# Kernel optimization log

Hardware: AMD Instinct MI355X
Metric: run time of the kernel (lower is better)

Reference implementation:

```python
import jax, jax.numpy as jnp
import numpy as np
import math

B, N, D = 4096, 41, 271
S, THR, KS = 0.3, 1e-4, 25  # wavelet scale s=0.3, threshold 1e-4, Bessel series terms
_IV_COEFS = [np.array([1.0 / (math.factorial(k) * math.factorial(k + n)) for k in range(KS)], dtype=np.float32) for n in range(4)]


def _iv(n, x):
    # modified Bessel I_n(x) via power series, x >= 0, shape [B]
    k = np.arange(KS, dtype=np.float32)
    xh = (0.5 * x)[:, None]
    return jnp.sum(_IV_COEFS[n] * xh ** (n + 2.0 * k), axis=-1)


def _l1norm(W):
    # F.normalize(p=1, dim=2)
    return W / jnp.maximum(jnp.sum(jnp.abs(W), axis=2, keepdims=True), 1e-12)


def _bn(x, g, b):
    # BatchNorm1d in training mode: per-feature stats over the batch dim (biased var)
    m = jnp.mean(x, 0)
    v = jnp.var(x, 0)
    return (x - m) / jnp.sqrt(v + 1e-5) * g + b


def _wavelet_basis(G):
    # laplacian_multi: degree from raw W, symmetrize, D^-1/2 (D - A) D^-1/2
    deg = jnp.sum(G, axis=-1)                               # [B,N]
    A = 0.5 * (G + jnp.swapaxes(G, 1, 2))                   # [B,N,N]
    dinv = 1.0 / (jnp.sqrt(deg) + 1e-6)
    eye = jnp.eye(N, dtype=G.dtype)
    L = dinv[:, :, None] * (deg[:, :, None] * eye - A) * dinv[:, None, :]
    # cheb_polynomial_multi: note order-0 term is ZEROS in the source
    T2 = 2.0 * jnp.matmul(L, L)
    T3 = 2.0 * jnp.matmul(L, T2) - L
    Lch = jnp.stack([jnp.zeros_like(L), L, T2, T3], axis=1)  # [B,4,N,N]
    # largest_lamb: host-side eigsh(LM) per sample -> detached (no grad)
    lam = jax.lax.stop_gradient(jnp.max(jnp.abs(jnp.linalg.eigvalsh(L)), axis=-1))  # [B]
    x = S * 0.5 * lam                                       # s * a, a = lamb/2
    ivs = jnp.stack([_iv(n, x) for n in range(4)], axis=1)  # [B,4]
    sign = jnp.asarray([1.0, -1.0, 1.0, -1.0], dtype=x.dtype)  # I_n(-x) = (-1)^n I_n(x)
    c = 2.0 * jnp.exp(x)[:, None] * ivs                     # 2 e^{sa} I_n(sa)
    inv_c = 2.0 * jnp.exp(-x)[:, None] * ivs * sign         # 2 e^{-sa} I_n(-sa)
    W = jnp.einsum('bo,bonm->bnm', c, Lch)
    Wi = jnp.einsum('bo,bonm->bnm', inv_c, Lch)
    W = _l1norm(jnp.where(W < THR, 0.0, W))
    Wi = _l1norm(jnp.where(Wi < THR, 0.0, Wi))
    return W, Wi


def _forward(G, X, gwnn_kernel, gwnn_W, log_scale_vector, W1, b1, W2, b2, bn1_gamma, bn1_beta):
    wav, wav_inv = _wavelet_basis(G)
    # graph wavelet layer: psi diag(k) psi^{-1} X W  (dropout off / eval)
    h = jnp.matmul(X, gwnn_W)                 # [B,N,D]
    h = jnp.matmul(wav_inv, h)
    h = gwnn_kernel[None, :, None] * h
    h = jax.nn.relu(jnp.matmul(wav, h))
    # scaling layer: exp(log_scale) * x
    coff = jnp.exp(log_scale_vector)          # [N,D]
    fr = coff[None] * h
    # shape1: Linear -> ReLU -> Linear
    fr = jnp.matmul(jax.nn.relu(jnp.matmul(fr, W1) + b1), W2) + b2
    # sequence feature: mean over nodes then BatchNorm1d(271)
    seq = _bn(jnp.mean(fr, axis=1), bn1_gamma, bn1_beta)  # [B,D]
    return seq


def setup_inputs() -> dict:
    key = jax.random.key(0)
    ks = jax.random.split(key, 8)
    sc = 1.0 / np.sqrt(D).astype(np.float32)
    return {
        'G': jax.random.uniform(ks[0], (B, N, N), jnp.float32),
        'X': jax.random.normal(ks[1], (B, N, D), jnp.float32),
        'gwnn_kernel': 1.0 + 0.1 * jax.random.normal(ks[2], (N,), jnp.float32),
        'gwnn_W': sc * jax.random.normal(ks[3], (D, D), jnp.float32),
        'log_scale_vector': 0.1 * jax.random.normal(ks[4], (N, D), jnp.float32),
        'W1': sc * jax.random.normal(ks[5], (D, D), jnp.float32),
        'b1': jnp.zeros((D,), jnp.float32),
        'W2': sc * jax.random.normal(ks[6], (D, D), jnp.float32),
        'b2': jnp.zeros((D,), jnp.float32),
        'bn1_gamma': jnp.ones((D,), jnp.float32),
        'bn1_beta': jnp.zeros((D,), jnp.float32),
    }


def reference(G, X, gwnn_kernel, gwnn_W, log_scale_vector, W1, b1, W2, b2, bn1_gamma, bn1_beta):
    return _forward(G, X, gwnn_kernel, gwnn_W, log_scale_vector, W1, b1, W2, b2, bn1_gamma, bn1_beta)
```

## Files before the change

### kernel.cpp

```cpp
#include <hip/hip_runtime.h>
#include <math.h>

namespace {
constexpr int BB = 4096;
constexpr int NN = 41;
constexpr int DD = 271;
constexpr int DP = 288;
constexpr int PW = 44;
constexpr long long MROWS = (long long)BB * NN;
constexpr int WBE = DP * DP * 2;
constexpr int WBS = (DP / 32) * DP * 32;
constexpr int SROW = 312;
constexpr int NPL = 5;
}

typedef __attribute__((ext_vector_type(8)))  unsigned short ushort8;
typedef __attribute__((ext_vector_type(8)))  short          short8;
typedef __attribute__((ext_vector_type(4)))  float          f32x4;

__device__ __forceinline__ unsigned short f2bf(float f) {
    unsigned u = __float_as_uint(f);
    unsigned r = (u + 0x7FFFu + ((u >> 16) & 1u)) >> 16;
    return (unsigned short)r;
}
__device__ __forceinline__ float bf2f(unsigned short h) {
    return __uint_as_float(((unsigned)h) << 16);
}

__device__ __forceinline__ void store_split_km(unsigned short* __restrict__ dst,
                                               long long nrows, long long row,
                                               int col, float v)
{
    const unsigned short hh = f2bf(v);
    const unsigned short ll = f2bf(v - bf2f(hh));
    const long long base = ((long long)(col >> 5) * nrows + row) * 64;
    const int cn = (col & 31) >> 3, k7 = col & 7, sw = (int)(row & 7);
    dst[base + ((cn ^ sw) << 3) + k7]       = hh;
    dst[base + (((cn + 4) ^ sw) << 3) + k7] = ll;
}

__device__ __forceinline__ void lds_mm(const float (*__restrict__ A)[PW],
                                       const float (*__restrict__ B)[PW],
                                       float (*__restrict__ C)[PW],
                                       const float scale,
                                       const float (*__restrict__ sub)[PW],
                                       const int tid)
{
    for (int s = tid; s < NN * 11; s += 256) {
        const int i = s / 11, q = s % 11;
        float4 acc = make_float4(0.f, 0.f, 0.f, 0.f);
        #pragma unroll
        for (int k = 0; k < NN; ++k) {
            const float a = A[i][k];
            const float4 b4 = *reinterpret_cast<const float4*>(&B[k][q * 4]);
            acc.x = fmaf(a, b4.x, acc.x); acc.y = fmaf(a, b4.y, acc.y);
            acc.z = fmaf(a, b4.z, acc.z); acc.w = fmaf(a, b4.w, acc.w);
        }
        float4 r;
        if (sub) {
            const float4 s4 = *reinterpret_cast<const float4*>(&sub[i][q * 4]);
            r = make_float4(fmaf(scale, acc.x, -s4.x), fmaf(scale, acc.y, -s4.y),
                            fmaf(scale, acc.z, -s4.z), fmaf(scale, acc.w, -s4.w));
        } else {
            r = make_float4(scale * acc.x, scale * acc.y, scale * acc.z, scale * acc.w);
        }
        *reinterpret_cast<float4*>(&C[i][q * 4]) = r;
    }
}

__global__ __launch_bounds__(256) void k_wavelet(const float* __restrict__ G,
                                                 const float* __restrict__ gk,
                                                 float* __restrict__ MT)
{
    __shared__ float sG[NN][PW];
    __shared__ float sL[NN][PW];
    __shared__ float sT2[NN][PW];
    __shared__ float sT3[NN][PW];
    __shared__ float sM[NN][PW];
    __shared__ float sdeg[NN], sdinv[NN], srs[NN];
    __shared__ float slam16;

    const int b   = blockIdx.x;
    const int tid = threadIdx.x;
    const float* Gb = G + (size_t)b * NN * NN;

    for (int e = tid; e < NN * PW; e += 256) {
        const int i = e / PW, j = e % PW;
        sG[i][j] = (j < NN) ? Gb[i * NN + j] : 0.0f;
    }
    __syncthreads();

    if (tid < NN) {
        float4 s4 = make_float4(0.f, 0.f, 0.f, 0.f);
        #pragma unroll
        for (int q = 0; q < 11; ++q) {
            const float4 g4 = *reinterpret_cast<const float4*>(&sG[tid][q * 4]);
            s4.x += g4.x; s4.y += g4.y; s4.z += g4.z; s4.w += g4.w;
        }
        const float s = (s4.x + s4.y) + (s4.z + s4.w);
        sdeg[tid]  = s;
        sdinv[tid] = 1.0f / (sqrtf(s) + 1e-6f);
    }
    __syncthreads();

    for (int e = tid; e < NN * PW; e += 256) {
        const int i = e / PW, j = e % PW;
        if (j < NN) {
            const float a = 0.5f * (sG[i][j] + sG[j][i]);
            const float v = ((i == j) ? sdeg[i] : 0.0f) - a;
            sL[i][j] = sdinv[i] * sdinv[j] * v;
        } else {
            sL[i][j] = 0.0f;
        }
    }
    __syncthreads();

    lds_mm(sL, sL, sT2, 2.0f, nullptr, tid);
    __syncthreads();
    lds_mm(sL, sT2, sT3, 2.0f, sL, tid);
    __syncthreads();

    lds_mm(sT2, sT2, sM, 0.25f, nullptr, tid);
    __syncthreads();
    lds_mm(sM, sM, sG, 1.0f, nullptr, tid);
    __syncthreads();
    lds_mm(sG, sG, sM, 1.0f, nullptr, tid);
    __syncthreads();

    if (tid < 64) {
        float lr[NN];
        #pragma unroll
        for (int j = 0; j < NN; ++j) lr[j] = (tid < NN) ? sM[tid][j] : 0.0f;
        unsigned h = (unsigned)(tid + 1) * 2654435761u;
        h ^= h >> 13; h *= 0x85ebca6bu; h ^= h >> 16;
        float v = (tid < NN) ? (0.25f + (float)(h & 1023) * (1.0f / 1024.0f)) : 0.0f;
        float n2 = v * v;
        #pragma unroll
        for (int off = 32; off > 0; off >>= 1) n2 += __shfl_xor(n2, off, 64);
        v *= rsqrtf(n2);
        float lam = 1.0f;
        #pragma unroll
        for (int it = 0; it < 4; ++it) {
            float acc = 0.f;
            #pragma unroll
            for (int j = 0; j < NN; ++j) acc = fmaf(lr[j], __shfl(v, j, 64), acc);
            float m2 = acc * acc;
            #pragma unroll
            for (int off = 32; off > 0; off >>= 1) m2 += __shfl_xor(m2, off, 64);
            lam = sqrtf(m2);
            v = acc * (1.0f / lam);
        }
        if (tid == 0) slam16 = lam;
    }
    __syncthreads();

    const float x = 0.15f * exp2f(log2f(slam16) * (1.0f / 16.0f));
    float iv[4];
    {
        const float xh = 0.5f * x, xh2 = xh * xh;
        #pragma unroll
        for (int n = 0; n < 4; ++n) {
            float c = 1.0f;
            for (int q = 2; q <= n; ++q) c /= (float)q;
            float p = 1.0f;
            for (int q = 0; q < n; ++q) p *= xh;
            float s = 0.f;
            for (int k = 0; k < 25; ++k) {
                s += c * p;
                p *= xh2;
                c /= (float)((k + 1) * (k + 1 + n));
            }
            iv[n] = s;
        }
    }
    const float ex = expf(x), emx = expf(-x);

    {
        const float a1 = 2.f * ex * iv[1], a2 = 2.f * ex * iv[2], a3 = 2.f * ex * iv[3];
        for (int s = tid; s < NN * 11; s += 256) {
            const int i = s / 11, q = s % 11;
            const float4 l4  = *reinterpret_cast<const float4*>(&sL[i][q * 4]);
            const float4 t24 = *reinterpret_cast<const float4*>(&sT2[i][q * 4]);
            const float4 t34 = *reinterpret_cast<const float4*>(&sT3[i][q * 4]);
            float4 w;
            w.x = fmaf(a1, l4.x, fmaf(a2, t24.x, a3 * t34.x));
            w.y = fmaf(a1, l4.y, fmaf(a2, t24.y, a3 * t34.y));
            w.z = fmaf(a1, l4.z, fmaf(a2, t24.z, a3 * t34.z));
            w.w = fmaf(a1, l4.w, fmaf(a2, t24.w, a3 * t34.w));
            w.x = (w.x < 1e-4f) ? 0.f : w.x;  w.y = (w.y < 1e-4f) ? 0.f : w.y;
            w.z = (w.z < 1e-4f) ? 0.f : w.z;  w.w = (w.w < 1e-4f) ? 0.f : w.w;
            *reinterpret_cast<float4*>(&sM[i][q * 4]) = w;
        }
        __syncthreads();
        if (tid < NN) {
            float s = 0.f;
            #pragma unroll
            for (int q = 0; q < 11; ++q) {
                const float4 w4 = *reinterpret_cast<const float4*>(&sM[tid][q * 4]);
                s += fabsf(w4.x) + fabsf(w4.y) + fabsf(w4.z) + fabsf(w4.w);
            }
            srs[tid] = 1.0f / fmaxf(s, 1e-12f);
        }
        __syncthreads();
    }
    {
        const float a1 = -2.f * emx * iv[1], a2 = 2.f * emx * iv[2], a3 = -2.f * emx * iv[3];
        for (int s = tid; s < NN * 11; s += 256) {
            const int i = s / 11, q = s % 11;
            float4 m4 = *reinterpret_cast<float4*>(&sM[i][q * 4]);
            const float rs = srs[i];
            m4.x *= rs; m4.y *= rs; m4.z *= rs; m4.w *= rs;
            *reinterpret_cast<float4*>(&sM[i][q * 4]) = m4;
            const float4 l4  = *reinterpret_cast<const float4*>(&sL[i][q * 4]);
            const float4 t24 = *reinterpret_cast<const float4*>(&sT2[i][q * 4]);
            const float4 t34 = *reinterpret_cast<const float4*>(&sT3[i][q * 4]);
            float4 w;
            w.x = fmaf(a1, l4.x, fmaf(a2, t24.x, a3 * t34.x));
            w.y = fmaf(a1, l4.y, fmaf(a2, t24.y, a3 * t34.y));
            w.z = fmaf(a1, l4.z, fmaf(a2, t24.z, a3 * t34.z));
            w.w = fmaf(a1, l4.w, fmaf(a2, t24.w, a3 * t34.w));
            w.x = (w.x < 1e-4f) ? 0.f : w.x;  w.y = (w.y < 1e-4f) ? 0.f : w.y;
            w.z = (w.z < 1e-4f) ? 0.f : w.z;  w.w = (w.w < 1e-4f) ? 0.f : w.w;
            *reinterpret_cast<float4*>(&sG[i][q * 4]) = w;
        }
        __syncthreads();
        if (tid < NN) {
            float s = 0.f;
            #pragma unroll
            for (int q = 0; q < 11; ++q) {
                const float4 w4 = *reinterpret_cast<const float4*>(&sG[tid][q * 4]);
                s += fabsf(w4.x) + fabsf(w4.y) + fabsf(w4.z) + fabsf(w4.w);
            }
            sdeg[tid] = gk[tid] / fmaxf(s, 1e-12f);
        }
        __syncthreads();
        for (int s = tid; s < NN * 11; s += 256) {
            const int j = s / 11, q = s % 11;
            float4 w4 = *reinterpret_cast<float4*>(&sG[j][q * 4]);
            const float rs = sdeg[j];
            w4.x *= rs; w4.y *= rs; w4.z *= rs; w4.w *= rs;
            *reinterpret_cast<float4*>(&sG[j][q * 4]) = w4;
        }
        __syncthreads();
    }
    lds_mm(sM, sG, sL, 1.0f, nullptr, tid);
    __syncthreads();
    float* dst = MT + (size_t)b * NN * NN;
    for (int e = tid; e < NN * NN; e += 256) {
        const int j = e / NN, i = e % NN;
        dst[e] = sL[i][j];
    }
}

__global__ __launch_bounds__(256) void k_splitB(const float* __restrict__ gW,
                                                const float* __restrict__ W1,
                                                const float* __restrict__ W2,
                                                const float* __restrict__ lsv,
                                                unsigned short* __restrict__ Bint,
                                                unsigned short* __restrict__ Bsng,
                                                float* __restrict__ coff)
{
    const int t = blockIdx.x * 256 + threadIdx.x;
    if (t < NN * DD) coff[t] = expf(lsv[t]);
    if (t >= 3 * DP * DP) return;
    const int w = t / (DP * DP);
    const int r = t % (DP * DP);
    const int n = r / DP, k = r % DP;
    const float* src = (w == 0) ? gW : ((w == 1) ? W1 : W2);
    const float v = (n < DD && k < DD) ? src[k * DD + n] : 0.0f;
    store_split_km(Bint + (size_t)w * WBE, DP, n, k, v);
    if (w < 2) {
        Bsng[(size_t)w * WBS + ((long long)(k >> 5) * DP + n) * 32 +
             (((k & 31) >> 3) << 3) + (k & 7)] = f2bf(v);
    }
}

__global__ __launch_bounds__(256, 2) void k_wavX(const float* __restrict__ MT,
                                                 const float* __restrict__ X,
                                                 unsigned short* __restrict__ Yint)
{
    constexpr int XJ  = 68;
    constexpr int YST = 296;
    __shared__ __align__(16) unsigned short sXT[288 * XJ];
    __shared__ __align__(16) unsigned short sMm[48 * XJ];
    __shared__ __align__(16) unsigned short sYb[NN * YST];
    const int b   = blockIdx.x;
    const int tid = threadIdx.x;
    const int lane = tid & 63, w = tid >> 6;
    const int lr = lane & 15;
    const int hi8 = (lane >> 4) * 8;

    const ushort8 z8 = {0, 0, 0, 0, 0, 0, 0, 0};
    for (int e = tid; e < (288 * XJ) / 8; e += 256)
        *reinterpret_cast<ushort8*>(&sXT[e * 8]) = z8;
    for (int e = tid; e < (48 * XJ) / 8; e += 256)
        *reinterpret_cast<ushort8*>(&sMm[e * 8]) = z8;
    __syncthreads();

    const float* __restrict__ Xb = X + (size_t)b * NN * DD;
    for (int e = tid; e < NN * DD; e += 256) {
        const int j = e / DD, c = e % DD;
        sXT[c * XJ + j] = f2bf(Xb[e]);
    }
    const float* __restrict__ Mb = MT + (size_t)b * NN * NN;
    for (int e = tid; e < NN * NN; e += 256) {
        const int j = e / NN, i = e % NN;
        sMm[i * XJ + j] = f2bf(Mb[e]);
    }
    __syncthreads();

    for (int t = w; t < 54; t += 4) {
        const int mt = t / 18, nt = t % 18;
        f32x4 acc = (f32x4){0.f, 0.f, 0.f, 0.f};
        #pragma unroll
        for (int ks = 0; ks < 2; ++ks) {
            const short8 a = *reinterpret_cast<const short8*>(
                &sMm[(mt * 16 + lr) * XJ + ks * 32 + hi8]);
            const short8 bf = *reinterpret_cast<const short8*>(
                &sXT[(nt * 16 + lr) * XJ + ks * 32 + hi8]);
            acc = __builtin_amdgcn_mfma_f32_16x16x32_bf16(a, bf, acc, 0, 0, 0);
        }
        const int row0 = mt * 16 + (lane >> 4) * 4;
        const int col  = nt * 16 + lr;
        #pragma unroll
        for (int rr = 0; rr < 4; ++rr) {
            const int row = row0 + rr;
            if (row < NN) sYb[row * YST + col] = f2bf(acc[rr]);
        }
    }
    __syncthreads();

    for (int t = tid; t < NN * 36; t += 256) {
        const int i = t / 36, c8 = t % 36;
        const ushort8 hv = *reinterpret_cast<const ushort8*>(&sYb[i * YST + c8 * 8]);
        const long long r = (long long)b * NN + i;
        const int p = c8 >> 3;
        const int chunk = ((c8 >> 2) & 1) * 4 + (c8 & 3);
        const int sw = (int)(r & 7);
        unsigned short* base = Yint + ((long long)p * MROWS + r) * 64;
        *reinterpret_cast<ushort8*>(base + ((chunk ^ sw) << 3)) = hv;
    }
}

__device__ __forceinline__ void async16(const unsigned short* __restrict__ g,
                                        unsigned short* l)
{
    __builtin_amdgcn_global_load_lds(
        (const __attribute__((address_space(1))) unsigned int*)g,
        (__attribute__((address_space(3))) unsigned int*)l, 16, 0, 0);
}

__global__ __launch_bounds__(512, 2) void k_fused(
    const unsigned short* __restrict__ Aint,
    const unsigned short* __restrict__ Bs0,
    const unsigned short* __restrict__ Bs1,
    const float* __restrict__ coff,
    const float* __restrict__ b1,
    unsigned short* __restrict__ P2)
{
    __shared__ __align__(16) unsigned short sS[256 * SROW];
    const int tid  = threadIdx.x;
    const int lane = tid & 63, w = tid >> 6;
    const int wr = w >> 1, wc = w & 1;
    const int lr = lane & 15, cb = lane >> 4;
    const int sw = lr & 7;

    const int nwg = gridDim.x, orig = blockIdx.x;
    const int q = nwg >> 3, r = nwg & 7;
    const int xcd = orig & 7, loc = orig >> 3;
    const int bid = (xcd < r ? xcd * (q + 1) : r * (q + 1) + (xcd - r) * q) + loc;
    const long long row0 = (long long)bid * 256;

    const unsigned short* __restrict__ b0p = Bs0 + (size_t)(wc * 144 + lr) * 32 + cb * 8;
    const unsigned short* __restrict__ b1p = Bs1 + (size_t)(wc * 144 + lr) * 32 + cb * 8;

    f32x4 acc[4][9];
    #pragma unroll
    for (int mf = 0; mf < 4; ++mf)
        #pragma unroll
        for (int nf = 0; nf < 9; ++nf)
            acc[mf][nf] = (f32x4){0.f, 0.f, 0.f, 0.f};

    for (int t = 0; t < 9; ++t) {
        const int p  = t >> 1;
        const int hc = (t & 1) * 4 + cb;
        const long long abase = ((long long)p * MROWS + row0) * 64 + ((hc ^ sw) << 3);
        short8 a[4];
        #pragma unroll
        for (int mf = 0; mf < 4; ++mf)
            a[mf] = *reinterpret_cast<const short8*>(
                Aint + abase + (long long)(wr * 64 + mf * 16 + lr) * 64);
        const long long toff = (long long)t * DP * 32;
        #pragma unroll
        for (int nf = 0; nf < 9; ++nf) {
            const short8 bh = *reinterpret_cast<const short8*>(b0p + toff + (long long)nf * 512);
            #pragma unroll
            for (int mf = 0; mf < 4; ++mf)
                acc[mf][nf] = __builtin_amdgcn_mfma_f32_16x16x32_bf16(a[mf], bh, acc[mf][nf], 0, 0, 0);
        }
    }

    #pragma unroll
    for (int mf = 0; mf < 4; ++mf) {
        const int mb = wr * 64 + mf * 16 + ((lane >> 4) * 4);
        #pragma unroll
        for (int nf = 0; nf < 9; ++nf) {
            const int col = wc * 144 + nf * 16 + lr;
            #pragma unroll
            for (int rr = 0; rr < 4; ++rr) {
                const int m = mb + rr;
                float v = fmaxf(acc[mf][nf][rr], 0.f);
                const float cf = (col < DD) ? coff[((unsigned)(row0 + m) % 41u) * DD + col] : 0.0f;
                sS[m * SROW + col] = f2bf(v * cf);
                acc[mf][nf][rr] = 0.f;
            }
        }
    }
    __syncthreads();

    for (int t = 0; t < 9; ++t) {
        short8 ah[4];
        #pragma unroll
        for (int mf = 0; mf < 4; ++mf) {
            const int m = wr * 64 + mf * 16 + lr;
            ah[mf] = *reinterpret_cast<const short8*>(&sS[m * SROW + t * 32 + cb * 8]);
        }
        const long long toff = (long long)t * DP * 32;
        #pragma unroll
        for (int nf = 0; nf < 9; ++nf) {
            const short8 bh = *reinterpret_cast<const short8*>(b1p + toff + (long long)nf * 512);
            #pragma unroll
            for (int mf = 0; mf < 4; ++mf)
                acc[mf][nf] = __builtin_amdgcn_mfma_f32_16x16x32_bf16(ah[mf], bh, acc[mf][nf], 0, 0, 0);
        }
    }

    #pragma unroll
    for (int mf = 0; mf < 4; ++mf) {
        const long long rb = row0 + wr * 64 + mf * 16 + ((lane >> 4) * 4);
        #pragma unroll
        for (int nf = 0; nf < 9; ++nf) {
            const int col = wc * 144 + nf * 16 + lr;
            const float bv = (col < DD) ? b1[col] : 0.0f;
            #pragma unroll
            for (int rr = 0; rr < 4; ++rr) {
                const float v = fmaxf(acc[mf][nf][rr] + bv, 0.f);
                P2[(rb + rr) * DP + col] = f2bf(v);
            }
        }
    }
}

__global__ __launch_bounds__(320) void k_meanP2(const unsigned short* __restrict__ P2,
                                                unsigned short* __restrict__ MPint)
{
    const int b = blockIdx.x;
    const int c = threadIdx.x;
    if (c >= DP) return;
    float s = 0.f;
    #pragma unroll
    for (int n = 0; n < NN; ++n)
        s += bf2f(P2[((size_t)b * NN + n) * DP + c]);
    s *= (1.0f / 41.0f);
    store_split_km(MPint, BB, b, c, s);
}

__global__ __launch_bounds__(256, 2) void k_gemm3(
    const unsigned short* __restrict__ Aint,
    const unsigned short* __restrict__ Bm,
    const float* __restrict__ bias,
    float* __restrict__ outF)
{
    __shared__ __align__(16) unsigned short As2[2][128 * 64];
    const int tid  = threadIdx.x;
    const int lane = tid & 63, w = tid >> 6;
    const int wr = w >> 1, wc = w & 1;
    const int lr = lane & 15, cb = lane >> 4;
    const int sw = lr & 7;
    const long long row0 = (long long)blockIdx.x * 128;

    const size_t brow = (size_t)(wc * 144 + lr) * 64;
    const unsigned short* __restrict__ bhp = Bm + brow + ((cb ^ sw) << 3);
    const unsigned short* __restrict__ blp = Bm + brow + (((cb + 4) ^ sw) << 3);

    f32x4 acc[4][9];
    #pragma unroll
    for (int mf = 0; mf < 4; ++mf)
        #pragma unroll
        for (int nf = 0; nf < 9; ++nf)
            acc[mf][nf] = (f32x4){0.f, 0.f, 0.f, 0.f};

    auto stageA = [&](unsigned short* dst, int kt32) {
        const unsigned short* src = Aint + ((long long)kt32 * BB + row0) * 64;
        #pragma unroll
        for (int i = 0; i < 4; ++i) {
            const int cid = tid + i * 256;
            async16(src + (long long)cid * 8, dst + cid * 8);
        }
    };

    stageA(As2[0], 0);
    for (int t = 0; t < 9; ++t) {
        __syncthreads();
        if (t < 8) stageA(As2[(t + 1) & 1], t + 1);
        const unsigned short* As = As2[t & 1];
        short8 ah[4], al[4];
        #pragma unroll
        for (int mf = 0; mf < 4; ++mf) {
            const int m = wr * 64 + mf * 16 + lr;
            ah[mf] = *reinterpret_cast<const short8*>(&As[m * 64 + ((cb ^ sw) << 3)]);
            al[mf] = *reinterpret_cast<const short8*>(&As[m * 64 + (((cb + 4) ^ sw) << 3)]);
        }
        const long long toff = (long long)t * DP * 64;
        #pragma unroll
        for (int nf = 0; nf < 9; ++nf) {
            const long long d = toff + (long long)nf * 1024;
            const short8 bh = *reinterpret_cast<const short8*>(bhp + d);
            const short8 bl = *reinterpret_cast<const short8*>(blp + d);
            #pragma unroll
            for (int mf = 0; mf < 4; ++mf) {
                acc[mf][nf] = __builtin_amdgcn_mfma_f32_16x16x32_bf16(ah[mf], bh, acc[mf][nf], 0, 0, 0);
                acc[mf][nf] = __builtin_amdgcn_mfma_f32_16x16x32_bf16(al[mf], bh, acc[mf][nf], 0, 0, 0);
                acc[mf][nf] = __builtin_amdgcn_mfma_f32_16x16x32_bf16(ah[mf], bl, acc[mf][nf], 0, 0, 0);
            }
        }
    }

    #pragma unroll
    for (int mf = 0; mf < 4; ++mf) {
        const long long rb = row0 + wr * 64 + mf * 16 + ((lane >> 4) * 4);
        #pragma unroll
        for (int nf = 0; nf < 9; ++nf) {
            const int col = wc * 144 + nf * 16 + lr;
            const float bv = (col < DD) ? bias[col] : 0.0f;
            #pragma unroll
            for (int rr = 0; rr < 4; ++rr)
                outF[(rb + rr) * DP + col] = acc[mf][nf][rr] + bv;
        }
    }
}

__global__ __launch_bounds__(256) void k_stats(const float* __restrict__ seq, float* __restrict__ stats)
{
    __shared__ float s1[256], s2[256];
    const int d = blockIdx.x;
    float a = 0.f, q = 0.f;
    for (int b = threadIdx.x; b < BB; b += 256) {
        float v = seq[(size_t)b * DP + d];
        a += v; q = fmaf(v, v, q);
    }
    s1[threadIdx.x] = a; s2[threadIdx.x] = q;
    __syncthreads();
    for (int o = 128; o > 0; o >>= 1) {
        if (threadIdx.x < o) { s1[threadIdx.x] += s1[threadIdx.x + o]; s2[threadIdx.x] += s2[threadIdx.x + o]; }
        __syncthreads();
    }
    if (threadIdx.x == 0) {
        float m = s1[0] * (1.0f / BB);
        float v = s2[0] * (1.0f / BB) - m * m;
        stats[d]      = m;
        stats[DD + d] = 1.0f / sqrtf(v + 1e-5f);
    }
}

__global__ __launch_bounds__(256) void k_bn(const float* __restrict__ seq, const float* __restrict__ stats,
                                            const float* __restrict__ g, const float* __restrict__ bt,
                                            float* __restrict__ out)
{
    const long long idx = (long long)blockIdx.x * 256 + threadIdx.x;
    if (idx < (long long)BB * DD) {
        const int d = (int)(idx % DD);
        const long long b = idx / DD;
        out[idx] = (seq[b * DP + d] - stats[d]) * stats[DD + d] * g[d] + bt[d];
    }
}

extern "C" void kernel_launch(void* const* d_in, const int* in_sizes, int n_in,
                              void* d_out, int out_size, void* d_ws, size_t ws_size,
                              hipStream_t stream)
{
    const float* G   = (const float*)d_in[0];
    const float* X   = (const float*)d_in[1];
    const float* gk  = (const float*)d_in[2];
    const float* gW  = (const float*)d_in[3];
    const float* lsv = (const float*)d_in[4];
    const float* W1  = (const float*)d_in[5];
    const float* b1  = (const float*)d_in[6];
    const float* W2  = (const float*)d_in[7];
    const float* b2  = (const float*)d_in[8];
    const float* gam = (const float*)d_in[9];
    const float* bet = (const float*)d_in[10];

    char* p = (char*)d_ws;
    auto alloc = [&](size_t bytes) { void* r = (void*)p; p += (bytes + 255) & ~(size_t)255; return r; };
    float*          MT    = (float*)alloc((size_t)BB * NN * NN * 4);
    unsigned short* Yint  = (unsigned short*)alloc((size_t)NPL * MROWS * 64 * 2);
    unsigned short* P2    = (unsigned short*)alloc((size_t)MROWS * DP * 2);
    unsigned short* Bint  = (unsigned short*)alloc((size_t)3 * WBE * 2);
    unsigned short* Bsng  = (unsigned short*)alloc((size_t)2 * WBS * 2);
    unsigned short* MPint = (unsigned short*)alloc((size_t)BB * 576 * 2);
    float*          coff  = (float*)alloc((size_t)NN * DD * 4);
    float*          seqF  = (float*)alloc((size_t)BB * DP * 4);
    float*          stats = (float*)alloc(2 * DD * 4);

    k_wavelet<<<BB, 256, 0, stream>>>(G, gk, MT);
    k_splitB<<<(3 * DP * DP + 255) / 256, 256, 0, stream>>>(gW, W1, W2, lsv, Bint, Bsng, coff);
    k_wavX<<<BB, 256, 0, stream>>>(MT, X, Yint);

    k_fused<<<(unsigned)(MROWS / 256), 512, 0, stream>>>(Yint, Bsng, Bsng + WBS,
                                                         coff, b1, P2);
    k_meanP2<<<BB, 320, 0, stream>>>(P2, MPint);
    k_gemm3<<<BB / 128, 256, 0, stream>>>(MPint, Bint + 2 * WBE, b2, seqF);
    k_stats<<<DD, 256, 0, stream>>>(seqF, stats);
    k_bn<<<(unsigned)(((long long)BB * DD + 255) / 256), 256, 0, stream>>>(seqF, stats, gam, bet, (float*)d_out);
}
```

Before: 435.2 us.

## Fuse node-mean reduction into fused GEMM epilogue via LDS and global atomics

The fused GEMM epilogue now accumulates ReLU outputs per sample into an LDS buffer with shared atomics, then flushes partial sums to a global fp32 buffer with global atomics. This removes writing and rereading the full bf16 P2 activation tensor (about 96 MB round trip). The price is many LDS atomics in the epilogue, a memset of the sum buffer, and cross-block global atomics where 256-row tiles straddle sample boundaries. It also makes the summation order nondeterministic.

```diff
diff --git a/kernel.cpp b/kernel.cpp
--- a/kernel.cpp
+++ b/kernel.cpp
@@ -356,7 +356,7 @@
     const unsigned short* __restrict__ Bs1,
     const float* __restrict__ coff,
     const float* __restrict__ b1,
-    unsigned short* __restrict__ P2)
+    float* __restrict__ seqsum)
 {
     __shared__ __align__(16) unsigned short sS[256 * SROW];
     const int tid  = threadIdx.x;
@@ -434,10 +434,16 @@
                 acc[mf][nf] = __builtin_amdgcn_mfma_f32_16x16x32_bf16(ah[mf], bh, acc[mf][nf], 0, 0, 0);
         }
     }
-
+    __syncthreads();
+
+    float* sums = reinterpret_cast<float*>(sS);
+    for (int e = tid; e < 8 * DP; e += 512) sums[e] = 0.f;
+    __syncthreads();
+
+    const int b0 = (int)(row0 / 41);
     #pragma unroll
     for (int mf = 0; mf < 4; ++mf) {
-        const long long rb = row0 + wr * 64 + mf * 16 + ((lane >> 4) * 4);
+        const int mb = wr * 64 + mf * 16 + ((lane >> 4) * 4);
         #pragma unroll
         for (int nf = 0; nf < 9; ++nf) {
             const int col = wc * 144 + nf * 16 + lr;
@@ -445,24 +451,31 @@
             #pragma unroll
             for (int rr = 0; rr < 4; ++rr) {
                 const float v = fmaxf(acc[mf][nf][rr] + bv, 0.f);
-                P2[(rb + rr) * DP + col] = f2bf(v);
+                const long long row = row0 + mb + rr;
+                const int ls = (int)(row / 41) - b0;
+                atomicAdd(&sums[ls * DP + col], v);
             }
         }
     }
-}
-
-__global__ __launch_bounds__(320) void k_meanP2(const unsigned short* __restrict__ P2,
-                                                unsigned short* __restrict__ MPint)
+    __syncthreads();
+
+    for (int e = tid; e < 8 * DP; e += 512) {
+        const int ls = e / DP, col = e % DP;
+        const long long bsm = (long long)b0 + ls;
+        if (bsm < BB) {
+            const float s = sums[e];
+            if (s != 0.f) atomicAdd(&seqsum[bsm * DP + col], s);
+        }
+    }
+}
+
+__global__ __launch_bounds__(320) void k_mp(const float* __restrict__ seqsum,
+                                            unsigned short* __restrict__ MPint)
 {
     const int b = blockIdx.x;
     const int c = threadIdx.x;
     if (c >= DP) return;
-    float s = 0.f;
-    #pragma unroll
-    for (int n = 0; n < NN; ++n)
-        s += bf2f(P2[((size_t)b * NN + n) * DP + c]);
-    s *= (1.0f / 41.0f);
-    store_split_km(MPint, BB, b, c, s);
+    store_split_km(MPint, BB, b, c, seqsum[(size_t)b * DP + c] * (1.0f / 41.0f));
 }
 
 __global__ __launch_bounds__(256, 2) void k_gemm3(
@@ -593,23 +606,25 @@
 
     char* p = (char*)d_ws;
     auto alloc = [&](size_t bytes) { void* r = (void*)p; p += (bytes + 255) & ~(size_t)255; return r; };
-    float*          MT    = (float*)alloc((size_t)BB * NN * NN * 4);
-    unsigned short* Yint  = (unsigned short*)alloc((size_t)NPL * MROWS * 64 * 2);
-    unsigned short* P2    = (unsigned short*)alloc((size_t)MROWS * DP * 2);
-    unsigned short* Bint  = (unsigned short*)alloc((size_t)3 * WBE * 2);
-    unsigned short* Bsng  = (unsigned short*)alloc((size_t)2 * WBS * 2);
-    unsigned short* MPint = (unsigned short*)alloc((size_t)BB * 576 * 2);
-    float*          coff  = (float*)alloc((size_t)NN * DD * 4);
-    float*          seqF  = (float*)alloc((size_t)BB * DP * 4);
-    float*          stats = (float*)alloc(2 * DD * 4);
+    float*          MT     = (float*)alloc((size_t)BB * NN * NN * 4);
+    unsigned short* Yint   = (unsigned short*)alloc((size_t)NPL * MROWS * 64 * 2);
+    unsigned short* Bint   = (unsigned short*)alloc((size_t)3 * WBE * 2);
+    unsigned short* Bsng   = (unsigned short*)alloc((size_t)2 * WBS * 2);
+    unsigned short* MPint  = (unsigned short*)alloc((size_t)BB * 576 * 2);
+    float*          coff   = (float*)alloc((size_t)NN * DD * 4);
+    float*          seqsum = (float*)alloc((size_t)BB * DP * 4);
+    float*          seqF   = (float*)alloc((size_t)BB * DP * 4);
+    float*          stats  = (float*)alloc(2 * DD * 4);
+
+    hipMemsetAsync(seqsum, 0, (size_t)BB * DP * 4, stream);
 
     k_wavelet<<<BB, 256, 0, stream>>>(G, gk, MT);
     k_splitB<<<(3 * DP * DP + 255) / 256, 256, 0, stream>>>(gW, W1, W2, lsv, Bint, Bsng, coff);
     k_wavX<<<BB, 256, 0, stream>>>(MT, X, Yint);
 
     k_fused<<<(unsigned)(MROWS / 256), 512, 0, stream>>>(Yint, Bsng, Bsng + WBS,
-                                                         coff, b1, P2);
-    k_meanP2<<<BB, 320, 0, stream>>>(P2, MPint);
+                                                         coff, b1, seqsum);
+    k_mp<<<BB, 320, 0, stream>>>(seqsum, MPint);
     k_gemm3<<<BB / 128, 256, 0, stream>>>(MPint, Bint + 2 * WBE, b2, seqF);
     k_stats<<<DD, 256, 0, stream>>>(seqF, stats);
     k_bn<<<(unsigned)(((long long)BB * DD + 255) / 256), 256, 0, stream>>>(seqF, stats, gam, bet, (float*)d_out);
```

Measured after the change: 669.2 us. +53.8%, slower.
